# Optimization experiments

Measured on AMD Instinct MI355X. Metric: run time of the kernel, lower is better.

Reference implementation:

```python
import jax, jax.numpy as jnp
import numpy as np

BITS = 8
BER = 1e-3
STRIDE = 1
PAD = 1


def _quant_ste(x, bits):
    # symmetric per-tensor fixed-point quantization (Quant in the original repo),
    # straight-through so backward is non-degenerate
    qmax = 2 ** (bits - 1) - 1
    scale = jnp.max(jnp.abs(jax.lax.stop_gradient(x))) / qmax + 1e-12
    q = jnp.clip(jnp.round(x / scale), -(qmax + 1), qmax) * scale
    return x + jax.lax.stop_gradient(q - x)


def _bitflip_fi(x, ber, bits, key):
    # operation_fi / operation_mulfi: quantize to `bits`-bit two's complement and
    # flip (at most) one uniformly chosen bit per element with prob ber*bits.
    qmax = 2 ** (bits - 1) - 1
    scale = jnp.max(jnp.abs(jax.lax.stop_gradient(x))) / qmax + 1e-12
    q = jnp.clip(jnp.round(x / scale), -(qmax + 1), qmax).astype(jnp.int32)
    qt = jnp.bitwise_and(q, 2 ** bits - 1)  # two's complement view
    k1, k2 = jax.random.split(key)
    u = jax.random.uniform(k1, x.shape)
    pos = jax.random.randint(k2, x.shape, 0, bits)
    mask = jnp.where(u < ber * bits, jnp.left_shift(jnp.int32(1), pos), 0)
    qf = jnp.bitwise_xor(qt, mask)
    qs = jnp.where(qf >= 2 ** (bits - 1), qf - 2 ** bits, qf).astype(x.dtype)
    y = qs * scale
    return x + jax.lax.stop_gradient(y - x)


def _unfold(x, kh, kw, pad, stride):
    # torch.nn.functional.unfold: output feature order is (C, kh, kw), C slowest
    B, C, H, W = x.shape
    oh = (H + 2 * pad - kh) // stride + 1
    ow = (W + 2 * pad - kw) // stride + 1
    xp = jnp.pad(x, ((0, 0), (0, 0), (pad, pad), (pad, pad)))
    cols = [xp[:, :, i:i + stride * oh:stride, j:j + stride * ow:stride]
            for i in range(kh) for j in range(kw)]
    unf = jnp.stack(cols, axis=2)  # [B, C, kh*kw, oh, ow]
    return unf.reshape(B, C * kh * kw, oh * ow), oh, ow


def setup_inputs() -> dict:
    key = jax.random.key(0)
    kx, kw = jax.random.split(key)
    x = jax.random.normal(kx, (1, 32, 56, 56), dtype=jnp.float32)
    weight = jax.random.normal(kw, (64, 32, 3, 3), dtype=jnp.float32) * 0.05
    return {"x": x, "weight": weight}


def reference(x, weight):
    key = jax.random.key(42)
    Co, Ci, kh, kw = weight.shape
    wq = _quant_ste(weight, BITS)
    unf, oh, ow = _unfold(x, kh, kw, PAD, STRIDE)      # [B, K, L], K=Ci*kh*kw
    xc = jnp.swapaxes(unf, 1, 2)                        # [B, L, K]
    wf = wq.reshape(Co, -1)                             # [Co, K]
    # broadcast elementwise products of every MAC term (the x1*w1 of the original)
    p = xc[:, None, :, :] * wf[None, :, None, :]        # [B, Co, L, K]
    k1, k2, k3 = jax.random.split(key, 3)
    p = _bitflip_fi(p, BER, BITS, k1)                   # operation_mulfi
    c = jnp.cumsum(p, axis=3)                           # running partial sums
    c_fi = _bitflip_fi(c, BER, BITS, k2)                # operation_fi on partial sums
    y_sum = c_fi[..., -1]
    c_error = (c_fi[..., 1:-1] - c[..., 1:-1]).sum(axis=3)  # injected-error fold-in
    y = y_sum + c_error                                 # [B, Co, L]
    y = _bitflip_fi(y, BER, BITS, k3)                   # operation_fi on outputs
    B = x.shape[0]
    return y.reshape(B, Co, oh, ow)
```

## Files before the change

kernel.cpp:

```cpp
#include <hip/hip_runtime.h>
#include <cstdint>

#define CO   64
#define CI   32
#define HH   56
#define WW   56
#define LL   3136
#define KK   288
#define KH   144
#define NOUT 200704u
#define KG   4
#define TO   32

#define FLIP_LT 34359808u

#define FCAP1 320
#define FCAP2 512

#define CWS_OFF_FLOATS 20480u
#define WS_NEED (81920ull + 4ull * 288ull * 200704ull)

__host__ __device__ inline uint32_t rotl32(uint32_t v, uint32_t r) {
#ifdef __HIP_DEVICE_COMPILE__
  return __builtin_amdgcn_alignbit(v, v, 32u - r);
#else
  return (v << r) | (v >> (32u - r));
#endif
}

__host__ __device__ inline void tf2x32(uint32_t k0, uint32_t k1,
                                       uint32_t x0, uint32_t x1,
                                       uint32_t& o0, uint32_t& o1) {
  uint32_t ks2 = k0 ^ k1 ^ 0x1BD11BDAu;
  uint32_t v0 = x0 + k0, v1 = x1 + k1;
#define TF_R(r) { v0 += v1; v1 = rotl32(v1, r); v1 ^= v0; }
  TF_R(13) TF_R(15) TF_R(26) TF_R(6)
  v0 += k1;  v1 += ks2 + 1u;
  TF_R(17) TF_R(29) TF_R(16) TF_R(24)
  v0 += ks2; v1 += k0 + 2u;
  TF_R(13) TF_R(15) TF_R(26) TF_R(6)
  v0 += k0;  v1 += k1 + 3u;
  TF_R(17) TF_R(29) TF_R(16) TF_R(24)
  v0 += k1;  v1 += ks2 + 4u;
  TF_R(13) TF_R(15) TF_R(26) TF_R(6)
  v0 += ks2; v1 += k0 + 5u;
#undef TF_R
  o0 = v0; o1 = v1;
}

__device__ inline uint32_t rbits(uint32_t k0, uint32_t k1, uint32_t i) {
  uint32_t o0, o1;
  tf2x32(k0, k1, 0u, i, o0, o1);
  return o0 ^ o1;
}

__device__ inline float qround(float xv, float scale, float rs) {
#pragma clang fp contract(off)
  float q0 = xv * rs;
  float er = fmaf(-scale, q0, xv);
  return rintf(fmaf(er, rs, q0));
}

__device__ inline float wquant(float wv, float scale_w) {
#pragma clang fp contract(off)
  float q = fminf(127.0f, fmaxf(-128.0f, rintf(wv / scale_w)));
  float y = q * scale_w;
  return wv + (y - wv);
}

__device__ inline float fi_fwd_skip(float x, float scale,
                                    uint32_t ub, uint32_t kp0, uint32_t kp1,
                                    uint32_t i0) {
#pragma clang fp contract(off)
  float q = rintf(x / scale);
  q = fminf(127.0f, fmaxf(-128.0f, q));
  bool flip = ub < FLIP_LT;
  float y;
  if (__any(flip)) {
    uint32_t pb = rbits(kp0, kp1, i0);
    uint32_t qt = ((uint32_t)(int)q) & 0xFFu;
    uint32_t mask = flip ? (1u << (pb & 7u)) : 0u;
    uint32_t qf = qt ^ mask;
    float qs = (float)(int)(signed char)(qf);
    y = qs * scale;
  } else {
    y = q * scale;
  }
  return x + (y - x);
}

template <int BS>
__device__ inline float block_max(float v) {
  __shared__ float s[BS];
  int t = threadIdx.x;
  __syncthreads();
  s[t] = v; __syncthreads();
  for (int o = BS / 2; o > 0; o >>= 1) {
    if (t < o) s[t] = fmaxf(s[t], s[t + o]);
    __syncthreads();
  }
  return s[0];
}

__global__ __launch_bounds__(256) void k_wmax(const float* __restrict__ w,
                                              unsigned int* __restrict__ mbits) {
  int i = blockIdx.x * 256 + threadIdx.x;
  float m = fabsf(w[i]);
  m = block_max<256>(m);
  if (threadIdx.x == 0) atomicMax(mbits, __float_as_uint(m));
}

__global__ __launch_bounds__(256) void k_maxp(const float* __restrict__ x,
                                              const float* __restrict__ w,
                                              const unsigned int* __restrict__ scal,
                                              unsigned int* __restrict__ maxp_bits) {
#pragma clang fp contract(off)
  int k = blockIdx.x;
  int ci = k / 9, r = k % 9, di = r / 3, dj = r % 3;
  const float* xr = x + ci * LL;
  float scale_w = __uint_as_float(scal[0]) / 127.0f + 1e-12f;
  float mx = 0.f;
  for (int l = threadIdx.x; l < LL; l += 256) {
    int oy = l / WW, ox = l % WW;
    int yy = oy + di - 1, xx = ox + dj - 1;
    float v = (yy >= 0 && yy < HH && xx >= 0 && xx < WW) ? xr[yy * WW + xx] : 0.f;
    mx = fmaxf(mx, fabsf(v));
  }
  float mw = 0.f;
  for (int co = threadIdx.x; co < CO; co += 256)
    mw = fmaxf(mw, fabsf(wquant(w[co * KK + k], scale_w)));
  mx = block_max<256>(mx);
  mw = block_max<256>(mw);
  if (threadIdx.x == 0) atomicMax(maxp_bits, __float_as_uint(mx * mw));
}

__global__ __launch_bounds__(256) void k_fi1cs(const float* __restrict__ x,
                                               const float* __restrict__ w,
                                               const unsigned int* __restrict__ scal,
                                               unsigned int* __restrict__ maxc_bits,
                                               float* __restrict__ cws,
                                               uint32_t ku0, uint32_t ku1,
                                               uint32_t kp0, uint32_t kp1) {
#pragma clang fp contract(off)
  __shared__ float sW[KK];
  __shared__ float sP[KH][TO];
  __shared__ uint32_t sCnt;
  __shared__ uint32_t sMeta[FCAP1];
  __shared__ float    sVal[FCAP1];
  int tid = threadIdx.x;
  uint32_t outi0 = blockIdx.x * (uint32_t)TO;
  int co = (int)(outi0 / (uint32_t)LL);
  float scale_w = __uint_as_float(scal[0]) / 127.0f + 1e-12f;
  for (int i = tid; i < KK; i += 256) sW[i] = wquant(w[co * KK + i], scale_w);
  if (tid == 0) sCnt = 0u;
  __syncthreads();

  int o = tid & 31, s = tid >> 5;
  uint32_t outi = outi0 + (uint32_t)o;
  int l = (int)(outi - (uint32_t)co * LL);
  int oy = l / WW, ox = l % WW;
  float scale_p = __uint_as_float(scal[1]) / 127.0f + 1e-12f;
  float rs_p = 1.0f / scale_p;
  uint32_t ibase = outi * (uint32_t)KK;

  float carry = 0.f, maxc = 0.f;
  for (int half = 0; half < 2; ++half) {
    int kbase = half * KH;
    int k = kbase + s * 18;
    int ci0 = k / 9;
    for (int c2 = 0; c2 < 2; ++c2) {
      const float* xr = x + (ci0 + c2) * LL;
      float xv[9];
      uint32_t ub[9];
#pragma unroll
      for (int di = 0; di < 3; ++di) {
        int yy = oy + di - 1;
        bool yok = (yy >= 0) && (yy < HH);
#pragma unroll
        for (int dj = 0; dj < 3; ++dj) {
          int xx = ox + dj - 1;
          xv[di * 3 + dj] = (yok && xx >= 0 && xx < WW) ? xr[yy * WW + xx] : 0.f;
        }
      }
#pragma unroll
      for (int j = 0; j < 9; ++j)
        ub[j] = rbits(ku0, ku1, ibase + (uint32_t)(k + j));
#pragma unroll
      for (int j = 0; j < 9; ++j) {
        float p = xv[j] * sW[k + j];
        float q = qround(p, scale_p, rs_p);
        float y = q * scale_p;
        sP[k + j - kbase][o] = p + (y - p);
        bool flip = ub[j] < FLIP_LT;
        if (__any(flip)) {
          if (flip) {
            uint32_t idx = atomicAdd(&sCnt, 1u);
            if (idx < FCAP1) {
              sMeta[idx] = ((uint32_t)(k + j) << 5) | (uint32_t)o;
              sVal[idx] = p;
            }
          }
        }
      }
      k += 9;
    }
    __syncthreads();
    {
      uint32_t n = sCnt; if (n > FCAP1) n = FCAP1;
      for (uint32_t i2 = (uint32_t)tid; i2 < n; i2 += 256u) {
        uint32_t meta = sMeta[i2];
        float p = sVal[i2];
        uint32_t kg = meta >> 5, oo = meta & 31u;
        uint32_t i0 = (outi0 + oo) * (uint32_t)KK + kg;
        uint32_t pb = rbits(kp0, kp1, i0);
        float q = qround(p, scale_p, rs_p);
        uint32_t qt = ((uint32_t)(int)q) & 0xFFu;
        uint32_t qf = qt ^ (1u << (pb & 7u));
        float qs = (float)(int)(signed char)(qf);
        float yv = qs * scale_p;
        sP[kg - (uint32_t)kbase][oo] = p + (yv - p);
      }
    }
    __syncthreads();
    if (tid < TO) {
      float c = carry;
#pragma unroll 8
      for (int kk = 0; kk < KH; ++kk) {
        c += sP[kk][tid];
        sP[kk][tid] = c;
        maxc = fmaxf(maxc, fabsf(c));
      }
      carry = c;
    }
    if (tid == 255) sCnt = 0u;
    __syncthreads();
    for (int b = s; b < 18; b += 8) {
      int gb = half * 18 + b;
      float4 v0 = {sP[b * 8 + 0][o], sP[b * 8 + 1][o],
                   sP[b * 8 + 2][o], sP[b * 8 + 3][o]};
      float4 v1 = {sP[b * 8 + 4][o], sP[b * 8 + 5][o],
                   sP[b * 8 + 6][o], sP[b * 8 + 7][o]};
      float* op = cws + ((size_t)gb * NOUT + outi) * 8u;
      *(float4*)op = v0;
      *((float4*)op + 1) = v1;
    }
    __syncthreads();
  }
  if (tid < 64) {
#pragma unroll
    for (int off = 32; off > 0; off >>= 1)
      maxc = fmaxf(maxc, __shfl_down(maxc, off));
    if (tid == 0) atomicMax(maxc_bits, __float_as_uint(maxc));
  }
}

__global__ __launch_bounds__(256) void k_fi2split(const float* __restrict__ cws,
                                                  const unsigned int* __restrict__ scal,
                                                  unsigned int* __restrict__ maxy_bits,
                                                  float* __restrict__ yout,
                                                  uint32_t ku0, uint32_t ku1,
                                                  uint32_t kp0, uint32_t kp1) {
#pragma clang fp contract(off)
  __shared__ float sE[KG][64];
  __shared__ float sYs[64];
  __shared__ float sEC[64];
  __shared__ float sYsC[64];
  __shared__ uint32_t sCnt;
  __shared__ uint32_t sMeta[FCAP2];
  __shared__ float    sVal[FCAP2];
  int tid = threadIdx.x;
  int lane = tid & 63;
  int kg = tid >> 6;
  if (tid < 64) { sEC[tid] = 0.f; sYsC[tid] = 0.f; }
  if (tid == 0) sCnt = 0u;
  __syncthreads();
  uint32_t outi = blockIdx.x * 64u + (uint32_t)lane;
  float scale_c = __uint_as_float(scal[2]) / 127.0f + 1e-12f;
  float rs_c = 1.0f / scale_c;
  uint32_t ibb = outi * (uint32_t)KK;
  const size_t BSTR = (size_t)NOUT * 8u;
  float e = 0.f;

  int b0 = kg * 9;
  const float* bp = cws + (size_t)outi * 8u + (size_t)b0 * BSTR;
  uint32_t ib = ibb + (uint32_t)(b0 * 8);
  uint32_t kbm = (uint32_t)(b0 * 8);
  for (int b = 0; b < 9; ++b) {
    float4 A  = *(const float4*)bp;
    float4 Bv = *(const float4*)(bp + 4);
    float c8[8] = {A.x, A.y, A.z, A.w, Bv.x, Bv.y, Bv.z, Bv.w};
    uint32_t ub[8];
#pragma unroll
    for (int j = 0; j < 8; ++j) ub[j] = rbits(ku0, ku1, ib + (uint32_t)j);
#pragma unroll
    for (int j = 0; j < 8; ++j) {
      float c = c8[j];
      float q = qround(c, scale_c, rs_c);
      float y = q * scale_c;
      float cf = c + (y - c);
      e += (cf - c);
      bool flip = ub[j] < FLIP_LT;
      if (__any(flip)) {
        if (flip) {
          uint32_t idx = atomicAdd(&sCnt, 1u);
          if (idx < FCAP2) {
            sMeta[idx] = ((kbm + (uint32_t)j) << 6) | (uint32_t)lane;
            sVal[idx] = c;
          }
        }
      }
    }
    bp += BSTR; ib += 8u; kbm += 8u;
  }

  float ys = 0.f;
  if (kg == 0) {
    float c0 = cws[(size_t)outi * 8u];
    float q = qround(c0, scale_c, rs_c);
    float y = q * scale_c;
    float cf = c0 + (y - c0);
    e -= (cf - c0);
  } else if (kg == KG - 1) {
    float c287 = cws[(size_t)outi * 8u + 35u * BSTR + 7u];
    float q = qround(c287, scale_c, rs_c);
    float y = q * scale_c;
    float cf = c287 + (y - c287);
    e -= (cf - c287);
    ys = cf;
  }
  sE[kg][lane] = e;
  if (kg == KG - 1) sYs[lane] = ys;
  __syncthreads();
  {
    uint32_t n = sCnt; if (n > FCAP2) n = FCAP2;
    for (uint32_t i2 = (uint32_t)tid; i2 < n; i2 += 256u) {
      uint32_t meta = sMeta[i2];
      float c = sVal[i2];
      uint32_t kx = meta >> 6, ln = meta & 63u;
      uint32_t i0 = (blockIdx.x * 64u + ln) * (uint32_t)KK + kx;
      uint32_t pb = rbits(kp0, kp1, i0);
      float q = qround(c, scale_c, rs_c);
      uint32_t qt = ((uint32_t)(int)q) & 0xFFu;
      uint32_t qf = qt ^ (1u << (pb & 7u));
      float qs = (float)(int)(signed char)(qf);
      float yf = qs * scale_c;
      float cff = c + (yf - c);
      float ysk = q * scale_c;
      float cfs = c + (ysk - c);
      float corr = cff - cfs;
      if (kx == 287u)     sYsC[ln] = corr;
      else if (kx != 0u)  atomicAdd(&sEC[ln], corr);
    }
  }
  __syncthreads();
  float maxy = 0.f;
  if (tid < 64) {
    float ee = ((sE[0][lane] + sE[1][lane]) + sE[2][lane]) + sE[3][lane];
    float y = (sYs[lane] + sYsC[lane]) + (ee + sEC[lane]);
    yout[outi] = y;
    maxy = fabsf(y);
  }
  maxy = block_max<256>(maxy);
  if (tid == 0) atomicMax(maxy_bits, __float_as_uint(maxy));
}

__global__ __launch_bounds__(64) void k_passC_nostore(const float* __restrict__ x,
                                                      const float* __restrict__ w,
                                                      const unsigned int* __restrict__ scal,
                                                      unsigned int* __restrict__ maxc_bits,
                                                      uint32_t ku0, uint32_t ku1,
                                                      uint32_t kp0, uint32_t kp1) {
#pragma clang fp contract(off)
  __shared__ float sW[KK];
  int co = blockIdx.y;
  float scale_w = __uint_as_float(scal[0]) / 127.0f + 1e-12f;
  for (int i = threadIdx.x; i < KK; i += 64) sW[i] = wquant(w[co * KK + i], scale_w);
  __syncthreads();
  int l = blockIdx.x * 64 + threadIdx.x;
  float maxc = 0.f;
  if (l < LL) {
    float scale_p = __uint_as_float(scal[1]) / 127.0f + 1e-12f;
    int oy = l / WW, ox = l % WW;
    uint32_t base = (uint32_t)(co * LL + l) * KK;
    float c = 0.f;
    int k = 0;
    for (int ci = 0; ci < CI; ++ci) {
      const float* xr = x + ci * LL;
#pragma unroll
      for (int di = 0; di < 3; ++di) {
        int yy = oy + di - 1;
        bool yok = (yy >= 0) && (yy < HH);
#pragma unroll
        for (int dj = 0; dj < 3; ++dj, ++k) {
          int xx = ox + dj - 1;
          float xv = (yok && xx >= 0 && xx < WW) ? xr[yy * WW + xx] : 0.f;
          float p = xv * sW[k];
          uint32_t i0 = base + (uint32_t)k;
          uint32_t ub = rbits(ku0, ku1, i0);
          c += fi_fwd_skip(p, scale_p, ub, kp0, kp1, i0);
          maxc = fmaxf(maxc, fabsf(c));
        }
      }
    }
  }
  maxc = block_max<64>(maxc);
  if (threadIdx.x == 0) atomicMax(maxc_bits, __float_as_uint(maxc));
}

__global__ __launch_bounds__(256) void k_passD_rec(const float* __restrict__ x,
                                                   const float* __restrict__ w,
                                                   const unsigned int* __restrict__ scal,
                                                   unsigned int* __restrict__ maxy_bits,
                                                   float* __restrict__ yout,
                                                   uint32_t ku10, uint32_t ku11,
                                                   uint32_t kp10, uint32_t kp11,
                                                   uint32_t ku20, uint32_t ku21,
                                                   uint32_t kp20, uint32_t kp21) {
#pragma clang fp contract(off)
  __shared__ float sW[KK];
  int co = blockIdx.y;
  float scale_w = __uint_as_float(scal[0]) / 127.0f + 1e-12f;
  for (int i = threadIdx.x; i < KK; i += 256) sW[i] = wquant(w[co * KK + i], scale_w);
  __syncthreads();
  int l = blockIdx.x * 256 + threadIdx.x;
  float maxy = 0.f;
  if (l < LL) {
    float scale_p = __uint_as_float(scal[1]) / 127.0f + 1e-12f;
    float scale_c = __uint_as_float(scal[2]) / 127.0f + 1e-12f;
    int oy = l / WW, ox = l % WW;
    uint32_t base = (uint32_t)(co * LL + l) * KK;
    float c = 0.f, e = 0.f, ys = 0.f;
    int k = 0;
    for (int ci = 0; ci < CI; ++ci) {
      const float* xr = x + ci * LL;
#pragma unroll
      for (int di = 0; di < 3; ++di) {
        int yy = oy + di - 1;
        bool yok = (yy >= 0) && (yy < HH);
#pragma unroll
        for (int dj = 0; dj < 3; ++dj, ++k) {
          int xx = ox + dj - 1;
          float xv = (yok && xx >= 0 && xx < WW) ? xr[yy * WW + xx] : 0.f;
          float p = xv * sW[k];
          uint32_t i0 = base + (uint32_t)k;
          uint32_t ub1 = rbits(ku10, ku11, i0);
          c += fi_fwd_skip(p, scale_p, ub1, kp10, kp11, i0);
          uint32_t ub2 = rbits(ku20, ku21, i0);
          float cf = fi_fwd_skip(c, scale_c, ub2, kp20, kp21, i0);
          if (k >= 1 && k <= 286) e += (cf - c);
          if (k == 287)           ys = cf;
        }
      }
    }
    float y = ys + e;
    yout[co * LL + l] = y;
    maxy = fabsf(y);
  }
  maxy = block_max<256>(maxy);
  if (threadIdx.x == 0) atomicMax(maxy_bits, __float_as_uint(maxy));
}

__global__ __launch_bounds__(256) void k_passE(float* __restrict__ y,
                                               const unsigned int* __restrict__ scal,
                                               uint32_t ku0, uint32_t ku1,
                                               uint32_t kp0, uint32_t kp1) {
#pragma clang fp contract(off)
  uint32_t i = blockIdx.x * 256u + threadIdx.x;
  float scale_y = __uint_as_float(scal[3]) / 127.0f + 1e-12f;
  uint32_t ub = rbits(ku0, ku1, i);
  y[i] = fi_fwd_skip(y[i], scale_y, ub, kp0, kp1, i);
}

extern "C" void kernel_launch(void* const* d_in, const int* in_sizes, int n_in,
                              void* d_out, int out_size, void* d_ws, size_t ws_size,
                              hipStream_t stream) {
  const float* x = (const float*)d_in[0];
  const float* w = (const float*)d_in[1];
  float* out = (float*)d_out;

  unsigned int* scal = (unsigned int*)d_ws;
  float* cws = (float*)d_ws + CWS_OFF_FLOATS;
  bool bigws = ws_size >= WS_NEED;

  uint32_t K1[2], K2[2], K3[2];
  tf2x32(0u, 42u, 0u, 0u, K1[0], K1[1]);
  tf2x32(0u, 42u, 0u, 1u, K2[0], K2[1]);
  tf2x32(0u, 42u, 0u, 2u, K3[0], K3[1]);
  auto derive = [](const uint32_t kk[2], uint32_t U[2], uint32_t P[2]) {
    uint32_t kA0, kA1, kB0, kB1, t0, t1;
    tf2x32(kk[0], kk[1], 0u, 0u, kA0, kA1);
    tf2x32(kk[0], kk[1], 0u, 1u, kB0, kB1);
    U[0] = kA0; U[1] = kA1;
    tf2x32(kB0, kB1, 0u, 1u, t0, t1);
    P[0] = t0; P[1] = t1;
  };
  uint32_t U1[2],P1[2],U2[2],P2[2],U3[2],P3[2];
  derive(K1, U1, P1); derive(K2, U2, P2); derive(K3, U3, P3);

  hipMemsetAsync(d_ws, 0, 64, stream);

  k_wmax<<<72, 256, 0, stream>>>(w, scal);
  k_maxp<<<KK, 256, 0, stream>>>(x, w, scal, scal + 1);
  if (bigws) {
    k_fi1cs<<<NOUT / TO, 256, 0, stream>>>(x, w, scal, scal + 2, cws,
                                           U1[0], U1[1], P1[0], P1[1]);
    k_fi2split<<<3136, 256, 0, stream>>>(cws, scal, scal + 3, out,
                                         U2[0], U2[1], P2[0], P2[1]);
  } else {
    dim3 gC(49, 64);
    k_passC_nostore<<<gC, 64, 0, stream>>>(x, w, scal, scal + 2,
                                           U1[0], U1[1], P1[0], P1[1]);
    dim3 gR(13, 64);
    k_passD_rec<<<gR, 256, 0, stream>>>(x, w, scal, scal + 3, out,
                                        U1[0], U1[1], P1[0], P1[1],
                                        U2[0], U2[1], P2[0], P2[1]);
  }
  k_passE<<<NOUT / 256, 256, 0, stream>>>(out, scal,
                                          U3[0], U3[1], P3[0], P3[1]);
}
```

Measured before the change: 349.7 us.

## Fold weight max into maxp kernel and regroup partial-sum workspace into 4-wide blocks

Removes the separate weight-abs-max kernel: every k_maxp block now recomputes the global weight max itself and block 0 writes it to the scalar slot. The partial-sum workspace changes from 8-float to 4-float interleaved blocks. k_fi2split now runs 32 outputs per block with 8 K-groups of 36 partials each, giving twice as many blocks and more threads per output. The trade is one fewer launch against redundant weight reads in every maxp block, narrower stores and loads, and a smaller flip buffer capacity per block.

```diff
diff --git a/kernel.cpp b/kernel.cpp
--- a/kernel.cpp
+++ b/kernel.cpp
@@ -9,13 +9,12 @@
 #define KK   288
 #define KH   144
 #define NOUT 200704u
-#define KG   4
 #define TO   32
 
 #define FLIP_LT 34359808u
 
 #define FCAP1 320
-#define FCAP2 512
+#define FCAP2 320
 
 #define CWS_OFF_FLOATS 20480u
 #define WS_NEED (81920ull + 4ull * 288ull * 200704ull)
@@ -102,23 +101,19 @@
   return s[0];
 }
 
-__global__ __launch_bounds__(256) void k_wmax(const float* __restrict__ w,
-                                              unsigned int* __restrict__ mbits) {
-  int i = blockIdx.x * 256 + threadIdx.x;
-  float m = fabsf(w[i]);
-  m = block_max<256>(m);
-  if (threadIdx.x == 0) atomicMax(mbits, __float_as_uint(m));
-}
-
 __global__ __launch_bounds__(256) void k_maxp(const float* __restrict__ x,
                                               const float* __restrict__ w,
-                                              const unsigned int* __restrict__ scal,
-                                              unsigned int* __restrict__ maxp_bits) {
-#pragma clang fp contract(off)
+                                              unsigned int* __restrict__ scal) {
+#pragma clang fp contract(off)
+  float mwall = 0.f;
+  for (int i = threadIdx.x; i < CO * KK; i += 256) mwall = fmaxf(mwall, fabsf(w[i]));
+  mwall = block_max<256>(mwall);
+  float scale_w = mwall / 127.0f + 1e-12f;
+  if (threadIdx.x == 0 && blockIdx.x == 0) scal[0] = __float_as_uint(mwall);
+
   int k = blockIdx.x;
   int ci = k / 9, r = k % 9, di = r / 3, dj = r % 3;
   const float* xr = x + ci * LL;
-  float scale_w = __uint_as_float(scal[0]) / 127.0f + 1e-12f;
   float mx = 0.f;
   for (int l = threadIdx.x; l < LL; l += 256) {
     int oy = l / WW, ox = l % WW;
@@ -131,7 +126,7 @@
     mw = fmaxf(mw, fabsf(wquant(w[co * KK + k], scale_w)));
   mx = block_max<256>(mx);
   mw = block_max<256>(mw);
-  if (threadIdx.x == 0) atomicMax(maxp_bits, __float_as_uint(mx * mw));
+  if (threadIdx.x == 0) atomicMax(scal + 1, __float_as_uint(mx * mw));
 }
 
 __global__ __launch_bounds__(256) void k_fi1cs(const float* __restrict__ x,
@@ -234,15 +229,12 @@
     }
     if (tid == 255) sCnt = 0u;
     __syncthreads();
-    for (int b = s; b < 18; b += 8) {
-      int gb = half * 18 + b;
-      float4 v0 = {sP[b * 8 + 0][o], sP[b * 8 + 1][o],
-                   sP[b * 8 + 2][o], sP[b * 8 + 3][o]};
-      float4 v1 = {sP[b * 8 + 4][o], sP[b * 8 + 5][o],
-                   sP[b * 8 + 6][o], sP[b * 8 + 7][o]};
-      float* op = cws + ((size_t)gb * NOUT + outi) * 8u;
+    for (int b = s; b < 36; b += 8) {
+      int gb = half * 36 + b;
+      float4 v0 = {sP[b * 4 + 0][o], sP[b * 4 + 1][o],
+                   sP[b * 4 + 2][o], sP[b * 4 + 3][o]};
+      float* op = cws + ((size_t)gb * NOUT + outi) * 4u;
       *(float4*)op = v0;
-      *((float4*)op + 1) = v1;
     }
     __syncthreads();
   }
@@ -261,40 +253,39 @@
                                                   uint32_t ku0, uint32_t ku1,
                                                   uint32_t kp0, uint32_t kp1) {
 #pragma clang fp contract(off)
-  __shared__ float sE[KG][64];
-  __shared__ float sYs[64];
-  __shared__ float sEC[64];
-  __shared__ float sYsC[64];
+  __shared__ float sE[8][TO];
+  __shared__ float sYs[TO];
+  __shared__ float sEC[TO];
+  __shared__ float sYsC[TO];
   __shared__ uint32_t sCnt;
   __shared__ uint32_t sMeta[FCAP2];
   __shared__ float    sVal[FCAP2];
   int tid = threadIdx.x;
-  int lane = tid & 63;
-  int kg = tid >> 6;
-  if (tid < 64) { sEC[tid] = 0.f; sYsC[tid] = 0.f; }
+  int o = tid & 31;
+  int kg = tid >> 5;
+  if (tid < TO) { sEC[tid] = 0.f; sYsC[tid] = 0.f; }
   if (tid == 0) sCnt = 0u;
   __syncthreads();
-  uint32_t outi = blockIdx.x * 64u + (uint32_t)lane;
+  uint32_t outi = blockIdx.x * (uint32_t)TO + (uint32_t)o;
   float scale_c = __uint_as_float(scal[2]) / 127.0f + 1e-12f;
   float rs_c = 1.0f / scale_c;
   uint32_t ibb = outi * (uint32_t)KK;
-  const size_t BSTR = (size_t)NOUT * 8u;
+  const size_t BSTR = (size_t)NOUT * 4u;
   float e = 0.f;
 
   int b0 = kg * 9;
-  const float* bp = cws + (size_t)outi * 8u + (size_t)b0 * BSTR;
-  uint32_t ib = ibb + (uint32_t)(b0 * 8);
-  uint32_t kbm = (uint32_t)(b0 * 8);
+  const float* bp = cws + (size_t)outi * 4u + (size_t)b0 * BSTR;
+  uint32_t ib = ibb + (uint32_t)(b0 * 4);
+  uint32_t kbm = (uint32_t)(b0 * 4);
   for (int b = 0; b < 9; ++b) {
-    float4 A  = *(const float4*)bp;
-    float4 Bv = *(const float4*)(bp + 4);
-    float c8[8] = {A.x, A.y, A.z, A.w, Bv.x, Bv.y, Bv.z, Bv.w};
-    uint32_t ub[8];
-#pragma unroll
-    for (int j = 0; j < 8; ++j) ub[j] = rbits(ku0, ku1, ib + (uint32_t)j);
-#pragma unroll
-    for (int j = 0; j < 8; ++j) {
-      float c = c8[j];
+    float4 A = *(const float4*)bp;
+    float c4[4] = {A.x, A.y, A.z, A.w};
+    uint32_t ub[4];
+#pragma unroll
+    for (int j = 0; j < 4; ++j) ub[j] = rbits(ku0, ku1, ib + (uint32_t)j);
+#pragma unroll
+    for (int j = 0; j < 4; ++j) {
+      float c = c4[j];
       float q = qround(c, scale_c, rs_c);
       float y = q * scale_c;
       float cf = c + (y - c);
@@ -304,40 +295,40 @@
         if (flip) {
           uint32_t idx = atomicAdd(&sCnt, 1u);
           if (idx < FCAP2) {
-            sMeta[idx] = ((kbm + (uint32_t)j) << 6) | (uint32_t)lane;
+            sMeta[idx] = ((kbm + (uint32_t)j) << 5) | (uint32_t)o;
             sVal[idx] = c;
           }
         }
       }
     }
-    bp += BSTR; ib += 8u; kbm += 8u;
+    bp += BSTR; ib += 4u; kbm += 4u;
   }
 
   float ys = 0.f;
   if (kg == 0) {
-    float c0 = cws[(size_t)outi * 8u];
+    float c0 = cws[(size_t)outi * 4u];
     float q = qround(c0, scale_c, rs_c);
     float y = q * scale_c;
     float cf = c0 + (y - c0);
     e -= (cf - c0);
-  } else if (kg == KG - 1) {
-    float c287 = cws[(size_t)outi * 8u + 35u * BSTR + 7u];
+  } else if (kg == 7) {
+    float c287 = cws[(size_t)outi * 4u + 71u * BSTR + 3u];
     float q = qround(c287, scale_c, rs_c);
     float y = q * scale_c;
     float cf = c287 + (y - c287);
     e -= (cf - c287);
     ys = cf;
   }
-  sE[kg][lane] = e;
-  if (kg == KG - 1) sYs[lane] = ys;
+  sE[kg][o] = e;
+  if (kg == 7) sYs[o] = ys;
   __syncthreads();
   {
     uint32_t n = sCnt; if (n > FCAP2) n = FCAP2;
     for (uint32_t i2 = (uint32_t)tid; i2 < n; i2 += 256u) {
       uint32_t meta = sMeta[i2];
       float c = sVal[i2];
-      uint32_t kx = meta >> 6, ln = meta & 63u;
-      uint32_t i0 = (blockIdx.x * 64u + ln) * (uint32_t)KK + kx;
+      uint32_t kx = meta >> 5, ln = meta & 31u;
+      uint32_t i0 = (blockIdx.x * (uint32_t)TO + ln) * (uint32_t)KK + kx;
       uint32_t pb = rbits(kp0, kp1, i0);
       float q = qround(c, scale_c, rs_c);
       uint32_t qt = ((uint32_t)(int)q) & 0xFFu;
@@ -354,9 +345,11 @@
   }
   __syncthreads();
   float maxy = 0.f;
-  if (tid < 64) {
-    float ee = ((sE[0][lane] + sE[1][lane]) + sE[2][lane]) + sE[3][lane];
-    float y = (sYs[lane] + sYsC[lane]) + (ee + sEC[lane]);
+  if (tid < TO) {
+    float ee = sE[0][o];
+#pragma unroll
+    for (int g = 1; g < 8; ++g) ee += sE[g][o];
+    float y = (sYs[o] + sYsC[o]) + (ee + sEC[o]);
     yout[outi] = y;
     maxy = fabsf(y);
   }
@@ -499,13 +492,12 @@
 
   hipMemsetAsync(d_ws, 0, 64, stream);
 
-  k_wmax<<<72, 256, 0, stream>>>(w, scal);
-  k_maxp<<<KK, 256, 0, stream>>>(x, w, scal, scal + 1);
+  k_maxp<<<KK, 256, 0, stream>>>(x, w, scal);
   if (bigws) {
     k_fi1cs<<<NOUT / TO, 256, 0, stream>>>(x, w, scal, scal + 2, cws,
                                            U1[0], U1[1], P1[0], P1[1]);
-    k_fi2split<<<3136, 256, 0, stream>>>(cws, scal, scal + 3, out,
-                                         U2[0], U2[1], P2[0], P2[1]);
+    k_fi2split<<<NOUT / TO, 256, 0, stream>>>(cws, scal, scal + 3, out,
+                                              U2[0], U2[1], P2[0], P2[1]);
   } else {
     dim3 gC(49, 64);
     k_passC_nostore<<<gC, 64, 0, stream>>>(x, w, scal, scal + 2,
```

Result: no change. 355.2 us (+1.6%).
